# Performance work log

Hardware: AMD Instinct MI355X
Metric: run time of the kernel (lower is better)

## Reference

```python
import jax, jax.numpy as jnp
import numpy as np

N_EMBD = 1024
N_HEADS = 16
HEAD_DIM = N_EMBD // N_HEADS


def setup_inputs() -> dict:
    key = jax.random.key(0)
    ks = jax.random.split(key, 5)
    s = 0.02
    return {
        "x": jax.random.normal(ks[0], (4, 2048, N_EMBD), dtype=jnp.float32),
        "w_attn": jax.random.normal(ks[1], (N_EMBD, 3 * N_EMBD), dtype=jnp.float32) * s,
        "b_attn": jnp.zeros((3 * N_EMBD,), dtype=jnp.float32),
        "w_proj": jax.random.normal(ks[2], (N_EMBD, N_EMBD), dtype=jnp.float32) * s,
        "b_proj": jnp.zeros((N_EMBD,), dtype=jnp.float32),
    }


def reference(x, w_attn, b_attn, w_proj, b_proj):
    B, T, C = x.shape
    H, D = N_HEADS, HEAD_DIM
    qkv = x @ w_attn + b_attn                      # [B,T,3C]
    q, k, v = jnp.split(qkv, 3, axis=-1)
    q = q.reshape(B, T, H, D).transpose(0, 2, 1, 3)  # [B,H,T,D]
    k = k.reshape(B, T, H, D).transpose(0, 2, 1, 3)
    v = v.reshape(B, T, H, D).transpose(0, 2, 1, 3)
    # Faithful to source bug: divide by d**(-0.5) == multiply by sqrt(d)
    scale = jnp.asarray(D, x.dtype) ** 0.5
    scores = jnp.einsum("bhqd,bhkd->bhqk", q, k) * scale  # [B,H,T,T]
    causal = jnp.tril(jnp.ones((T, T), dtype=bool))
    scores = jnp.where(causal[None, None], scores, -jnp.inf)
    attn = jax.nn.softmax(scores, axis=-1)
    y = jnp.einsum("bhqk,bhkd->bhqd", attn, v)     # [B,H,T,D]
    y = y.transpose(0, 2, 1, 3).reshape(B, T, C)
    return y @ w_proj + b_proj
```

## Files before the change

### kernel.cpp

```cpp
#include <hip/hip_runtime.h>
#include <cmath>

#define BB 4
#define TT 2048
#define CC 1024
#define HH 16
#define DD 64
#define MM (BB*TT)

typedef _Float16 f16x8 __attribute__((ext_vector_type(8)));
typedef _Float16 f16x4 __attribute__((ext_vector_type(4)));
typedef _Float16 f16x2 __attribute__((ext_vector_type(2)));
typedef float f32x4 __attribute__((ext_vector_type(4)));
typedef unsigned short ushort_t;

#define MFMA16(a,b,c) __builtin_amdgcn_mfma_f32_16x16x16f16(a,b,c,0,0,0)

__device__ __forceinline__ unsigned short f2h(float f) {
    _Float16 h = (_Float16)f;
    return __builtin_bit_cast(unsigned short, h);
}

__device__ __forceinline__ f16x2 cvt_pk(float a, float b) {
    return __builtin_bit_cast(f16x2, __builtin_amdgcn_cvt_pkrtz(a, b));
}

__device__ __forceinline__ void gld16(const void* gsrc, void* ldst) {
    void* g = const_cast<void*>(gsrc);
    __builtin_amdgcn_global_load_lds(
        (__attribute__((address_space(1))) void*)g,
        (__attribute__((address_space(3))) void*)ldst,
        16, 0, 0);
}

__global__ __launch_bounds__(256)
void cvt4_kernel(const float* __restrict__ in, ushort_t* __restrict__ out, long n4) {
    long i = (long)blockIdx.x * blockDim.x + threadIdx.x;
    if (i >= n4) return;
    float4 v = ((const float4*)in)[i];
    ushort4 o;
    o.x = f2h(v.x); o.y = f2h(v.y); o.z = f2h(v.z); o.w = f2h(v.w);
    ((ushort4*)out)[i] = o;
}

__global__ __launch_bounds__(256)
void trcvt2_kernel(const float* __restrict__ wa, const float* __restrict__ wp,
                   ushort_t* __restrict__ oa, ushort_t* __restrict__ op) {
    __shared__ float T[32][33];
    const int K = 1024;
    const float* in;
    ushort_t* out;
    int N, n0;
    if (blockIdx.x < 96) { in = wa; out = oa; N = 3072; n0 = blockIdx.x * 32; }
    else                 { in = wp; out = op; N = 1024; n0 = (blockIdx.x - 96) * 32; }
    const int tx = threadIdx.x & 31;
    const int ty = threadIdx.x >> 5;
    const int k0 = blockIdx.y * 32;
    #pragma unroll
    for (int i = 0; i < 4; ++i)
        T[ty + i * 8][tx] = in[(size_t)(k0 + ty + i * 8) * N + n0 + tx];
    __syncthreads();
    #pragma unroll
    for (int i = 0; i < 4; ++i)
        out[(size_t)(n0 + ty + i * 8) * K + k0 + tx] = f2h(T[tx][ty + i * 8]);
}

template<int N, bool QKV>
__global__ __launch_bounds__(256)
void hgemm_kernel(const ushort_t* __restrict__ A, const ushort_t* __restrict__ Bt,
                  const float* __restrict__ bias, float* __restrict__ out,
                  ushort_t* __restrict__ qh, ushort_t* __restrict__ kh,
                  ushort_t* __restrict__ vh)
{
    const int K = 1024;
    __shared__ ushort_t LDSU[16384];

    const int tid  = threadIdx.x;
    const int lane = tid & 63;
    const int wave = tid >> 6;
    const int wm   = (wave & 1) * 64;
    const int wn   = (wave >> 1) * 64;
    const int lrow = lane & 15;
    const int quad = lane >> 4;

    const int gx  = gridDim.x;
    const int nwg = gx * gridDim.y;
    int bid = blockIdx.y * gx + blockIdx.x;
    bid = (bid & 7) * (nwg >> 3) + (bid >> 3);
    const int m0 = (bid / gx) * 128;
    const int n0 = (bid % gx) * 128;

    unsigned offA[4], offB[4];
    ushort_t* ldsA[4];
    ushort_t* ldsB[4];
    #pragma unroll
    for (int p = 0; p < 4; ++p) {
        const int d   = p * 256 + tid;
        const int blk = d >> 9;
        const int row = (d >> 2) & 127;
        const int c16 = d & 3;
        offA[p] = (unsigned)(m0 + row) * K + blk * 32 + c16 * 8;
        offB[p] = (unsigned)(n0 + row) * K + blk * 32 + c16 * 8;
        ldsA[p] = &LDSU[0]    + (p * 256 + wave * 64) * 8;
        ldsB[p] = &LDSU[8192] + (p * 256 + wave * 64) * 8;
    }

    f32x4 acc[4][4];
    const f32x4 z = {0.f, 0.f, 0.f, 0.f};
    #pragma unroll
    for (int mt = 0; mt < 4; ++mt)
        #pragma unroll
        for (int nt = 0; nt < 4; ++nt)
            acc[mt][nt] = z;

    for (int kk = 0; kk < K; kk += 64) {
        #pragma unroll
        for (int p = 0; p < 4; ++p) {
            gld16(&A[offA[p] + kk],  ldsA[p]);
            gld16(&Bt[offB[p] + kk], ldsB[p]);
        }
        __syncthreads();

        #pragma unroll
        for (int ks = 0; ks < 2; ++ks) {
            f16x8 af[4], bf[4];
            #pragma unroll
            for (int mt = 0; mt < 4; ++mt)
                af[mt] = *(const f16x8*)&LDSU[ks * 4096 + (wm + mt * 16 + lrow) * 32 + quad * 8];
            #pragma unroll
            for (int nt = 0; nt < 4; ++nt)
                bf[nt] = *(const f16x8*)&LDSU[8192 + ks * 4096 + (wn + nt * 16 + lrow) * 32 + quad * 8];
            #pragma unroll
            for (int mt = 0; mt < 4; ++mt)
                #pragma unroll
                for (int nt = 0; nt < 4; ++nt)
                    acc[mt][nt] = __builtin_amdgcn_mfma_f32_16x16x32_f16(
                        af[mt], bf[nt], acc[mt][nt], 0, 0, 0);
        }
        __syncthreads();
    }

    if (QKV) {
        ushort_t* scr = &LDSU[wave * 4096];
        const int colw  = n0 + wn;
        const int which = colw >> 10;
        const int hh    = (colw & 1023) >> 6;
        const int rowt  = m0 + wm;
        const int b2    = rowt >> 11;
        const int t0w   = rowt & 2047;
        if (which == 2) {
            #pragma unroll
            for (int mt = 0; mt < 4; ++mt)
                #pragma unroll
                for (int nt = 0; nt < 4; ++nt) {
                    const float bv = bias[colw + nt * 16 + lrow];
                    f16x4 pk;
                    #pragma unroll
                    for (int r = 0; r < 4; ++r)
                        pk[r] = (_Float16)(acc[mt][nt][r] + bv);
                    *(f16x4*)&scr[(nt * 16 + lrow) * 64 + mt * 16 + quad * 4] = pk;
                }
            asm volatile("s_waitcnt lgkmcnt(0)" ::: "memory");
            ushort_t* base = vh + ((size_t)b2 * HH + hh) * DD * TT + t0w;
            #pragma unroll
            for (int it = 0; it < 8; ++it) {
                const int g  = it * 64 + lane;
                const int dd = g >> 3, cc = (g & 7) * 8;
                *(uint4*)&base[(size_t)dd * TT + cc] = *(const uint4*)&scr[dd * 64 + cc];
            }
        } else {
            const float sc = which ? 1.0f : 8.0f * 1.44269504088896f;
            #pragma unroll
            for (int mt = 0; mt < 4; ++mt)
                #pragma unroll
                for (int nt = 0; nt < 4; ++nt) {
                    const float bv = bias[colw + nt * 16 + lrow];
                    #pragma unroll
                    for (int r = 0; r < 4; ++r)
                        scr[(mt * 16 + quad * 4 + r) * 64 + nt * 16 + lrow] =
                            f2h((acc[mt][nt][r] + bv) * sc);
                }
            asm volatile("s_waitcnt lgkmcnt(0)" ::: "memory");
            ushort_t* dstp = (which ? kh : qh) +
                             (((size_t)b2 * HH + hh) * TT + t0w) * DD;
            #pragma unroll
            for (int it = 0; it < 8; ++it) {
                const int g = it * 64 + lane;
                *(uint4*)&dstp[g * 8] = *(const uint4*)&scr[g * 8];
            }
        }
    } else {
        #pragma unroll
        for (int mt = 0; mt < 4; ++mt) {
            const int rbase = m0 + wm + mt * 16 + quad * 4;
            #pragma unroll
            for (int nt = 0; nt < 4; ++nt) {
                const int col = n0 + wn + nt * 16 + lrow;
                const float bv = bias[col];
                #pragma unroll
                for (int r = 0; r < 4; ++r)
                    out[(size_t)(rbase + r) * N + col] = acc[mt][nt][r] + bv;
            }
        }
    }
}

__global__ __launch_bounds__(512, 4)
void attn_mfma_kernel(const ushort_t* __restrict__ qh, const ushort_t* __restrict__ kh,
                      const ushort_t* __restrict__ vh, ushort_t* __restrict__ yh)
{
    __shared__ ushort_t Ks[2][64 * 72];
    __shared__ ushort_t Vs[2][64 * 72];

    const int pr   = blockIdx.x;
    const int bh   = blockIdx.y;
    const int qtA  = 15 - pr;
    const int qtB  = pr;
    const int itA  = 2 * qtA + 2;
    const int tid  = threadIdx.x;
    const int lane = tid & 63;
    const int w    = tid >> 6;
    const int lrow = lane & 15;
    const int quad = lane >> 4;

    const ushort_t* qbase = qh + (size_t)bh * TT * DD;
    const ushort_t* kbase = kh + (size_t)bh * TT * DD;
    const ushort_t* vbase = vh + (size_t)bh * DD * TT;
    const int b = bh >> 4, h = bh & 15;

    const int ur = tid >> 3;
    const int uc = (tid & 7) * 8;

    int q0w = qtA * 128 + w * 16;
    f16x8 aq0 = *(const f16x8*)&qbase[(size_t)(q0w + lrow) * DD + quad * 8];
    f16x8 aq1 = *(const f16x8*)&qbase[(size_t)(q0w + lrow) * DD + 32 + quad * 8];

    const f32x4 z = {0.f, 0.f, 0.f, 0.f};
    f32x4 o[4] = {z, z, z, z};
    float mi = -1e30f, li = 0.f;

    uint4 kr = *(const uint4*)&kbase[(size_t)ur * DD + uc];
    uint4 vr = *(const uint4*)&vbase[(size_t)ur * TT + uc];

    *(uint4*)&Ks[0][ur * 72 + uc] = kr;
    *(uint4*)&Vs[0][ur * 72 + uc] = vr;
    kr = *(const uint4*)&kbase[(size_t)(64 + ur) * DD + uc];
    vr = *(const uint4*)&vbase[(size_t)ur * TT + 64 + uc];
    __syncthreads();

    for (int i = 0; i < 34; ++i) {
        const int cur = i & 1;
        if (i == itA) {
            #pragma unroll
            for (int r = 0; r < 4; ++r) {
                const float inv = 1.0f / __shfl(li, quad * 4 + r, 64);
                const int t = q0w + quad * 4 + r;
                #pragma unroll
                for (int dt = 0; dt < 4; ++dt)
                    yh[((size_t)b * TT + t) * CC + h * 64 + dt * 16 + lrow] =
                        f2h(o[dt][r] * inv);
            }
            q0w = qtB * 128 + w * 16;
            aq0 = *(const f16x8*)&qbase[(size_t)(q0w + lrow) * DD + quad * 8];
            aq1 = *(const f16x8*)&qbase[(size_t)(q0w + lrow) * DD + 32 + quad * 8];
            #pragma unroll
            for (int dt = 0; dt < 4; ++dt) o[dt] = z;
            mi = -1e30f; li = 0.f;
        }
        const int kt = (i < itA) ? i : i - itA;
        const int kt2 = kt * 64;
        if (kt2 <= q0w + 15) {
            f32x4 sv[4];
            __builtin_amdgcn_s_setprio(1);
            #pragma unroll
            for (int c = 0; c < 4; ++c) {
                f16x8 ka = *(const f16x8*)&Ks[cur][(c * 16 + lrow) * 72 + quad * 8];
                f16x8 kb = *(const f16x8*)&Ks[cur][(c * 16 + lrow) * 72 + 32 + quad * 8];
                sv[c] = __builtin_amdgcn_mfma_f32_16x16x32_f16(ka, aq0, z, 0, 0, 0);
                sv[c] = __builtin_amdgcn_mfma_f32_16x16x32_f16(kb, aq1, sv[c], 0, 0, 0);
            }
            __builtin_amdgcn_s_setprio(0);

            const int qg = q0w + lrow;
            if (kt2 + 63 > q0w) {
                #pragma unroll
                for (int c = 0; c < 4; ++c)
                    #pragma unroll
                    for (int r = 0; r < 4; ++r)
                        if (kt2 + c * 16 + quad * 4 + r > qg) sv[c][r] = -3e38f;
            }
            float mc[4];
            #pragma unroll
            for (int c = 0; c < 4; ++c)
                mc[c] = fmaxf(fmaxf(sv[c][0], sv[c][1]), fmaxf(sv[c][2], sv[c][3]));
            float m = fmaxf(fmaxf(mc[0], mc[1]), fmaxf(mc[2], mc[3]));
            m = fmaxf(m, __shfl_xor(m, 16, 64));
            m = fmaxf(m, __shfl_xor(m, 32, 64));

            if (__any(m > mi + 8.0f)) {
                const float mnew  = fmaxf(mi, m);
                const float alpha = exp2f(mi - mnew);
                mi = mnew;
                li *= alpha;
                #pragma unroll
                for (int r = 0; r < 4; ++r) {
                    const float ar = __shfl(alpha, quad * 4 + r, 64);
                    #pragma unroll
                    for (int dt = 0; dt < 4; ++dt) o[dt][r] *= ar;
                }
            }

            f16x4 ap[4];
            float rc[4];
            #pragma unroll
            for (int c = 0; c < 4; ++c) {
                const float p0 = exp2f(sv[c][0] - mi);
                const float p1 = exp2f(sv[c][1] - mi);
                const float p2 = exp2f(sv[c][2] - mi);
                const float p3 = exp2f(sv[c][3] - mi);
                rc[c] = (p0 + p1) + (p2 + p3);
                const f16x2 lo = cvt_pk(p0, p1);
                const f16x2 hi = cvt_pk(p2, p3);
                ap[c][0] = lo[0]; ap[c][1] = lo[1]; ap[c][2] = hi[0]; ap[c][3] = hi[1];
            }
            float rs = (rc[0] + rc[1]) + (rc[2] + rc[3]);
            rs += __shfl_xor(rs, 16, 64);
            rs += __shfl_xor(rs, 32, 64);
            li += rs;

            __builtin_amdgcn_s_setprio(1);
            #pragma unroll
            for (int dt = 0; dt < 4; ++dt)
                #pragma unroll
                for (int c = 0; c < 4; ++c) {
                    f16x4 vb = *(const f16x4*)&Vs[cur][(dt * 16 + lrow) * 72 + c * 16 + quad * 4];
                    o[dt] = MFMA16(ap[c], vb, o[dt]);
                }
            __builtin_amdgcn_s_setprio(0);
        }

        if (i < 33) {
            const int nxt = cur ^ 1;
            *(uint4*)&Ks[nxt][ur * 72 + uc] = kr;
            *(uint4*)&Vs[nxt][ur * 72 + uc] = vr;
            if (i < 32) {
                const int ni  = i + 2;
                const int nkt = (ni < itA) ? ni : ni - itA;
                const int nb  = nkt * 64;
                kr = *(const uint4*)&kbase[(size_t)(nb + ur) * DD + uc];
                vr = *(const uint4*)&vbase[(size_t)ur * TT + nb + uc];
            }
        }
        __syncthreads();
    }

    #pragma unroll
    for (int r = 0; r < 4; ++r) {
        const float inv = 1.0f / __shfl(li, quad * 4 + r, 64);
        const int t = q0w + quad * 4 + r;
        #pragma unroll
        for (int dt = 0; dt < 4; ++dt)
            yh[((size_t)b * TT + t) * CC + h * 64 + dt * 16 + lrow] =
                f2h(o[dt][r] * inv);
    }
}

extern "C" void kernel_launch(void* const* d_in, const int* in_sizes, int n_in,
                              void* d_out, int out_size, void* d_ws, size_t ws_size,
                              hipStream_t stream) {
    const float* x      = (const float*)d_in[0];
    const float* w_attn = (const float*)d_in[1];
    const float* b_attn = (const float*)d_in[2];
    const float* w_proj = (const float*)d_in[3];
    const float* b_proj = (const float*)d_in[4];
    float* out = (float*)d_out;

    const size_t per = (size_t)BB * HH * TT * DD;
    ushort_t* qh  = (ushort_t*)d_ws;
    ushort_t* kh  = qh + per;
    ushort_t* vh  = kh + per;
    ushort_t* xh  = vh + per;
    ushort_t* yh  = xh;
    ushort_t* wat = xh + (size_t)MM * CC;
    ushort_t* wpt = wat + (size_t)3 * CC * CC;

    cvt4_kernel<<<(MM * CC / 4 + 255) / 256, 256, 0, stream>>>(x, xh, MM * CC / 4);
    trcvt2_kernel<<<dim3(128, 32), 256, 0, stream>>>(w_attn, w_proj, wat, wpt);

    hgemm_kernel<3 * CC, true><<<dim3(3 * CC / 128, MM / 128), 256, 0, stream>>>(
        xh, wat, b_attn, nullptr, qh, kh, vh);

    attn_mfma_kernel<<<dim3(8, BB * HH), 512, 0, stream>>>(qh, kh, vh, yh);

    hgemm_kernel<CC, false><<<dim3(CC / 128, MM / 128), 256, 0, stream>>>(
        yh, wpt, b_proj, out, nullptr, nullptr, nullptr);
}
```

Baseline: 270.0 us.

## Add 256x256-tile QKV GEMM with triple-buffered direct-to-LDS loads

Result: slower. 286.9 us (+6.3%).

```diff
diff --git a/kernel.cpp b/kernel.cpp
--- a/kernel.cpp
+++ b/kernel.cpp
@@ -65,12 +65,167 @@
         out[(size_t)(n0 + ty + i * 8) * K + k0 + tx] = f2h(T[tx][ty + i * 8]);
 }
 
-template<int N, bool QKV>
+__global__ __launch_bounds__(512, 2)
+void hgemm8_kernel(const ushort_t* __restrict__ A, const ushort_t* __restrict__ Bt,
+                   const float* __restrict__ bias,
+                   ushort_t* __restrict__ qh, ushort_t* __restrict__ kh,
+                   ushort_t* __restrict__ vh)
+{
+    extern __shared__ ushort_t LDS[];
+
+    const int tid  = threadIdx.x;
+    const int lane = tid & 63;
+    const int wid  = tid >> 6;
+    const int wm   = wid >> 2;
+    const int wn   = wid & 3;
+    const int lrow = lane & 15;
+    const int quad = lane >> 4;
+
+    int bid = blockIdx.x;
+    bid = (bid & 7) * 48 + (bid >> 3);
+    const int m0 = (bid / 12) * 256;
+    const int n0 = (bid % 12) * 256;
+
+    const int rr = lane >> 2;
+    const int cc = ((lane & 3) * 8) ^ ((lane & 32) ? 16 : 0);
+    const unsigned gA0 = (unsigned)(m0 +       wid * 16 + rr) * 1024 + cc;
+    const unsigned gA1 = (unsigned)(m0 + 128 + wid * 16 + rr) * 1024 + cc;
+    const unsigned gB0 = (unsigned)(n0 +       wid * 16 + rr) * 1024 + cc;
+    const unsigned gB1 = (unsigned)(n0 + 128 + wid * 16 + rr) * 1024 + cc;
+
+    const int swz  = (lrow & 8) ? 16 : 0;
+    const int rdA0 = wm * 4096 + lrow * 32 + ((quad * 8) ^ swz);
+    const int rdB0 = 8192 + (wn >> 1) * 4096 +
+                     ((wn & 1) * 64 + lrow) * 32 + ((quad * 8) ^ swz);
+
+    f32x4 acc[8][4];
+    const f32x4 z = {0.f, 0.f, 0.f, 0.f};
+    #pragma unroll
+    for (int im = 0; im < 8; ++im)
+        #pragma unroll
+        for (int in = 0; in < 4; ++in)
+            acc[im][in] = z;
+
+    auto STAGE = [&](int t2, int hf) {
+        ushort_t* dst = &LDS[(t2 % 3) * 16384 + ((hf >= 2) ? 8192 : 0) +
+                             (hf & 1) * 4096 + wid * 512];
+        const unsigned go = (hf == 0 ? gA0 : hf == 1 ? gA1 : hf == 2 ? gB0 : gB1)
+                            + (unsigned)t2 * 32;
+        gld16((hf >= 2 ? Bt : A) + go, dst);
+    };
+
+    f16x8 af[4], bf[4];
+
+#define LDA_Q(QM) { _Pragma("unroll") \
+    for (int mt = 0; mt < 4; ++mt) \
+        af[mt] = *(const f16x8*)&LDS[ctb + rdA0 + ((QM) * 4 + mt) * 512]; }
+#define LDB_J(JN) { bf[JN] = *(const f16x8*)&LDS[ctb + rdB0 + (JN) * 512]; }
+#define DO_MFMA(QM, QN) { \
+    __builtin_amdgcn_s_setprio(1); \
+    _Pragma("unroll") \
+    for (int mt = 0; mt < 4; ++mt) \
+        _Pragma("unroll") \
+        for (int nt = 0; nt < 2; ++nt) \
+            acc[(QM) * 4 + mt][(QN) * 2 + nt] = \
+                __builtin_amdgcn_mfma_f32_16x16x32_f16( \
+                    af[mt], bf[(QN) * 2 + nt], acc[(QM) * 4 + mt][(QN) * 2 + nt], \
+                    0, 0, 0); \
+    __builtin_amdgcn_s_setprio(0); }
+
+    #pragma unroll
+    for (int hf = 0; hf < 4; ++hf) STAGE(0, hf);
+    #pragma unroll
+    for (int hf = 0; hf < 4; ++hf) STAGE(1, hf);
+    asm volatile("s_waitcnt vmcnt(4)" ::: "memory");
+    __builtin_amdgcn_s_barrier();
+
+    for (int t = 0; t < 32; ++t) {
+        const int ctb = (t % 3) * 16384;
+        const bool st = (t < 30);
+        LDA_Q(0); LDB_J(0); LDB_J(1);
+        if (st) STAGE(t + 2, 0);
+        __builtin_amdgcn_s_barrier();
+        DO_MFMA(0, 0);
+        __builtin_amdgcn_s_barrier();
+        LDB_J(2); LDB_J(3);
+        if (st) STAGE(t + 2, 1);
+        __builtin_amdgcn_s_barrier();
+        DO_MFMA(0, 1);
+        __builtin_amdgcn_s_barrier();
+        LDA_Q(1);
+        if (st) STAGE(t + 2, 2);
+        __builtin_amdgcn_s_barrier();
+        DO_MFMA(1, 1);
+        __builtin_amdgcn_s_barrier();
+        if (st) STAGE(t + 2, 3);
+        if (t < 30) asm volatile("s_waitcnt vmcnt(4)" ::: "memory");
+        else        asm volatile("s_waitcnt vmcnt(0)" ::: "memory");
+        __builtin_amdgcn_s_barrier();
+        DO_MFMA(1, 0);
+        __builtin_amdgcn_s_barrier();
+    }
+#undef LDA_Q
+#undef LDB_J
+#undef DO_MFMA
+
+    ushort_t* scr = &LDS[wid * 4096];
+    const int colw  = n0 + wn * 64;
+    const int which = colw >> 10;
+    const int hh    = (colw & 1023) >> 6;
+    const int rowt  = m0 + wm * 128;
+    const int b2    = rowt >> 11;
+    const int t0w   = rowt & 2047;
+    #pragma unroll
+    for (int ch = 0; ch < 2; ++ch) {
+        if (ch) asm volatile("s_waitcnt lgkmcnt(0)" ::: "memory");
+        if (which == 2) {
+            #pragma unroll
+            for (int mt = 0; mt < 4; ++mt)
+                #pragma unroll
+                for (int in = 0; in < 4; ++in) {
+                    const float bv = bias[colw + in * 16 + lrow];
+                    f16x4 pk;
+                    #pragma unroll
+                    for (int r = 0; r < 4; ++r)
+                        pk[r] = (_Float16)(acc[ch * 4 + mt][in][r] + bv);
+                    *(f16x4*)&scr[(in * 16 + lrow) * 64 + mt * 16 + quad * 4] = pk;
+                }
+            asm volatile("s_waitcnt lgkmcnt(0)" ::: "memory");
+            ushort_t* base = vh + ((size_t)b2 * HH + hh) * DD * TT + t0w + ch * 64;
+            #pragma unroll
+            for (int it = 0; it < 8; ++it) {
+                const int g  = it * 64 + lane;
+                const int dd = g >> 3, c2 = (g & 7) * 8;
+                *(uint4*)&base[(size_t)dd * TT + c2] = *(const uint4*)&scr[dd * 64 + c2];
+            }
+        } else {
+            const float sc = which ? 1.0f : 8.0f * 1.44269504088896f;
+            #pragma unroll
+            for (int mt = 0; mt < 4; ++mt)
+                #pragma unroll
+                for (int in = 0; in < 4; ++in) {
+                    const float bv = bias[colw + in * 16 + lrow];
+                    #pragma unroll
+                    for (int r = 0; r < 4; ++r)
+                        scr[(mt * 16 + quad * 4 + r) * 64 + in * 16 + lrow] =
+                            f2h((acc[ch * 4 + mt][in][r] + bv) * sc);
+                }
+            asm volatile("s_waitcnt lgkmcnt(0)" ::: "memory");
+            ushort_t* dstp = (which ? kh : qh) +
+                             ((size_t)(b2 * HH + hh) * TT + t0w + ch * 64) * DD;
+            #pragma unroll
+            for (int it = 0; it < 8; ++it) {
+                const int g = it * 64 + lane;
+                *(uint4*)&dstp[g * 8] = *(const uint4*)&scr[g * 8];
+            }
+        }
+    }
+}
+
+template<int N>
 __global__ __launch_bounds__(256)
 void hgemm_kernel(const ushort_t* __restrict__ A, const ushort_t* __restrict__ Bt,
-                  const float* __restrict__ bias, float* __restrict__ out,
-                  ushort_t* __restrict__ qh, ushort_t* __restrict__ kh,
-                  ushort_t* __restrict__ vh)
+                  const float* __restrict__ bias, float* __restrict__ out)
 {
     const int K = 1024;
     __shared__ ushort_t LDSU[16384];
@@ -140,67 +295,16 @@
         __syncthreads();
     }
 
-    if (QKV) {
-        ushort_t* scr = &LDSU[wave * 4096];
-        const int colw  = n0 + wn;
-        const int which = colw >> 10;
-        const int hh    = (colw & 1023) >> 6;
-        const int rowt  = m0 + wm;
-        const int b2    = rowt >> 11;
-        const int t0w   = rowt & 2047;
-        if (which == 2) {
-            #pragma unroll
-            for (int mt = 0; mt < 4; ++mt)
-                #pragma unroll
-                for (int nt = 0; nt < 4; ++nt) {
-                    const float bv = bias[colw + nt * 16 + lrow];
-                    f16x4 pk;
-                    #pragma unroll
-                    for (int r = 0; r < 4; ++r)
-                        pk[r] = (_Float16)(acc[mt][nt][r] + bv);
-                    *(f16x4*)&scr[(nt * 16 + lrow) * 64 + mt * 16 + quad * 4] = pk;
-                }
-            asm volatile("s_waitcnt lgkmcnt(0)" ::: "memory");
-            ushort_t* base = vh + ((size_t)b2 * HH + hh) * DD * TT + t0w;
-            #pragma unroll
-            for (int it = 0; it < 8; ++it) {
-                const int g  = it * 64 + lane;
-                const int dd = g >> 3, cc = (g & 7) * 8;
-                *(uint4*)&base[(size_t)dd * TT + cc] = *(const uint4*)&scr[dd * 64 + cc];
-            }
-        } else {
-            const float sc = which ? 1.0f : 8.0f * 1.44269504088896f;
-            #pragma unroll
-            for (int mt = 0; mt < 4; ++mt)
-                #pragma unroll
-                for (int nt = 0; nt < 4; ++nt) {
-                    const float bv = bias[colw + nt * 16 + lrow];
-                    #pragma unroll
-                    for (int r = 0; r < 4; ++r)
-                        scr[(mt * 16 + quad * 4 + r) * 64 + nt * 16 + lrow] =
-                            f2h((acc[mt][nt][r] + bv) * sc);
-                }
-            asm volatile("s_waitcnt lgkmcnt(0)" ::: "memory");
-            ushort_t* dstp = (which ? kh : qh) +
-                             (((size_t)b2 * HH + hh) * TT + t0w) * DD;
-            #pragma unroll
-            for (int it = 0; it < 8; ++it) {
-                const int g = it * 64 + lane;
-                *(uint4*)&dstp[g * 8] = *(const uint4*)&scr[g * 8];
-            }
-        }
-    } else {
+    #pragma unroll
+    for (int mt = 0; mt < 4; ++mt) {
+        const int rbase = m0 + wm + mt * 16 + quad * 4;
         #pragma unroll
-        for (int mt = 0; mt < 4; ++mt) {
-            const int rbase = m0 + wm + mt * 16 + quad * 4;
-            #pragma unroll
-            for (int nt = 0; nt < 4; ++nt) {
-                const int col = n0 + wn + nt * 16 + lrow;
-                const float bv = bias[col];
-                #pragma unroll
-                for (int r = 0; r < 4; ++r)
-                    out[(size_t)(rbase + r) * N + col] = acc[mt][nt][r] + bv;
-            }
+        for (int nt = 0; nt < 4; ++nt) {
+            const int col = n0 + wn + nt * 16 + lrow;
+            const float bv = bias[col];
+            #pragma unroll
+            for (int r = 0; r < 4; ++r)
+                out[(size_t)(rbase + r) * N + col] = acc[mt][nt][r] + bv;
         }
     }
 }
@@ -387,11 +491,11 @@
     cvt4_kernel<<<(MM * CC / 4 + 255) / 256, 256, 0, stream>>>(x, xh, MM * CC / 4);
     trcvt2_kernel<<<dim3(128, 32), 256, 0, stream>>>(w_attn, w_proj, wat, wpt);
 
-    hgemm_kernel<3 * CC, true><<<dim3(3 * CC / 128, MM / 128), 256, 0, stream>>>(
-        xh, wat, b_attn, nullptr, qh, kh, vh);
+    hgemm8_kernel<<<dim3(384), 512, 98304, stream>>>(
+        xh, wat, b_attn, qh, kh, vh);
 
     attn_mfma_kernel<<<dim3(8, BB * HH), 512, 0, stream>>>(qh, kh, vh, yh);
 
-    hgemm_kernel<CC, false><<<dim3(CC / 128, MM / 128), 256, 0, stream>>>(
-        yh, wpt, b_proj, out, nullptr, nullptr, nullptr);
-}
+    hgemm_kernel<CC><<<dim3(CC / 128, MM / 128), 256, 0, stream>>>(
+        yh, wpt, b_proj, out);
+}
```
